# Optimization experiments

Hardware: AMD Instinct MI355X
Metric: run time of the kernel (lower is better)

Reference implementation:

```python
import jax, jax.numpy as jnp
import numpy as np

B, N, CIN, COUT, K, E = 8, 50000, 64, 64, 3, 400000


def setup_inputs() -> dict:
    key = jax.random.key(0)
    k0, k1, k2, k3 = jax.random.split(key, 4)
    x = jax.random.normal(k0, (B, N, CIN), dtype=jnp.float32)
    weight = jax.random.normal(k1, (K, CIN, COUT), dtype=jnp.float32) * 0.05
    bias = jax.random.normal(k2, (COUT,), dtype=jnp.float32) * 0.05
    edge_index = jax.random.randint(k3, (2, E), 0, N, dtype=jnp.int64)
    return {"x": x, "weight": weight, "bias": bias, "edge_index": edge_index}


def reference(x, weight, bias, edge_index):
    b, n, cin = x.shape
    k_order = weight.shape[0]
    row, col = edge_index[0], edge_index[1]
    # remove self loops (edge_weight defaults to ones)
    ew = jnp.where(row != col, jnp.float32(1.0), jnp.float32(0.0))
    deg = jax.ops.segment_sum(ew, row, num_segments=n)
    dinv = jnp.where(deg > 0, deg ** -0.5, 0.0)
    lap = -dinv[row] * ew * dinv[col]  # [E]

    def prop(t):  # sparse lap @ t along node dim; t: [B, N, Cin]
        tn = t.transpose(1, 0, 2).reshape(n, -1)            # [N, B*Cin]
        y = jax.ops.segment_sum(lap[:, None] * tn[col], row, num_segments=n)
        return y.reshape(n, b, cin).transpose(1, 0, 2)       # [B, N, Cin]

    tx0 = x
    out = jnp.einsum('bni,io->bno', tx0, weight[0])
    if k_order > 1:
        tx1 = prop(x)
        out = out + jnp.einsum('bni,io->bno', tx1, weight[1])
    for k in range(2, k_order):
        tx2 = 2.0 * prop(tx1) - tx0
        out = out + jnp.einsum('bni,io->bno', tx2, weight[k])
        tx0, tx1 = tx1, tx2
    return out + bias
```

## Files before the change

kernel.cpp:

```cpp
#include <hip/hip_runtime.h>

#define NB 8
#define NN 50000
#define NC 64
#define NE 400000

typedef unsigned short us4 __attribute__((ext_vector_type(4)));
typedef unsigned short us8 __attribute__((ext_vector_type(8)));
typedef short s8v __attribute__((ext_vector_type(8)));
typedef float f4v __attribute__((ext_vector_type(4)));

__device__ __forceinline__ float bf2f(unsigned short u) {
  union { unsigned int i; float f; } v; v.i = ((unsigned int)u) << 16; return v.f;
}
__device__ __forceinline__ unsigned short f2bf(float f) {
  union { float f; unsigned int i; } v; v.f = f;
  unsigned int x = v.i;
  return (unsigned short)((x + 0x7FFFu + ((x >> 16) & 1u)) >> 16);
}
__device__ __forceinline__ void fma4(float4& a, float s, const float4& v) {
  a.x = fmaf(s, v.x, a.x); a.y = fmaf(s, v.y, a.y);
  a.z = fmaf(s, v.z, a.z); a.w = fmaf(s, v.w, a.w);
}

__device__ __forceinline__ void gather_group(
    const unsigned short* __restrict__ tb, const int2* __restrict__ edges,
    int s, int e, int lane, int2 myed, float (&acc)[8]) {
  int jc = s;
  while (jc < e) {
    int take = e - jc; if (take > 64) take = 64;
    if (jc != s) myed = edges[jc + (lane < take ? lane : take - 1)];
    int full = take & ~7;
    int m = 0;
    for (; m < full; m += 8) {
      us8 v[8]; float lp[8];
#pragma unroll
      for (int u = 0; u < 8; ++u) {
        int c = __shfl(myed.x, m + u, 64);
        lp[u] = __int_as_float(__shfl(myed.y, m + u, 64));
        v[u] = *(const us8*)&tb[(size_t)c * 512];
      }
#pragma unroll
      for (int u = 0; u < 8; ++u)
#pragma unroll
        for (int q = 0; q < 8; ++q) acc[q] = fmaf(lp[u], bf2f(v[u][q]), acc[q]);
    }
    if (m < take) {
      int rem = take - m;
      us8 v[8]; float lp[8];
#pragma unroll
      for (int u = 0; u < 8; ++u) {
        if (u < rem) {
          int c = __shfl(myed.x, m + u, 64);
          lp[u] = __int_as_float(__shfl(myed.y, m + u, 64));
          v[u] = *(const us8*)&tb[(size_t)c * 512];
        }
      }
#pragma unroll
      for (int u = 0; u < 8; ++u) {
        if (u < rem) {
#pragma unroll
          for (int q = 0; q < 8; ++q) acc[q] = fmaf(lp[u], bf2f(v[u][q]), acc[q]);
        }
      }
    }
    jc += take;
  }
}

__global__ void cheb_count(const int* __restrict__ ei, int* __restrict__ cnt) {
  int e = blockIdx.x * blockDim.x + threadIdx.x;
  if (e >= NE) return;
  int r = ei[e], c = ei[NE + e];
  if (r != c) atomicAdd(&cnt[r], 1);
}

__global__ void cheb_offsets(const int* __restrict__ cnt, float* __restrict__ dinv,
                             int* __restrict__ rowptr, int* __restrict__ cur,
                             int* __restrict__ total) {
  int n = blockIdx.x * blockDim.x + threadIdx.x;
  int lane = threadIdx.x & 63;
  bool valid = n < NN;
  int c = valid ? cnt[n] : 0;
  int inc = c;
#pragma unroll
  for (int d = 1; d < 64; d <<= 1) {
    int t = __shfl_up(inc, d, 64);
    if (lane >= d) inc += t;
  }
  int wtot = __shfl(inc, 63, 64);
  int base = 0;
  if (lane == 63) base = atomicAdd(total, wtot);
  base = __shfl(base, 63, 64);
  int s = base + inc - c;
  if (valid) {
    dinv[n] = (c > 0) ? rsqrtf((float)c) : 0.0f;
    rowptr[n] = s;
    cur[n] = s;
  }
}

__global__ void cheb_scatter(const int* __restrict__ ei, const float* __restrict__ dinv,
                             int* __restrict__ cur, int2* __restrict__ edges) {
  int e = blockIdx.x * blockDim.x + threadIdx.x;
  if (e >= NE) return;
  int r = ei[e], c = ei[NE + e];
  if (r == c) return;
  int pos = atomicAdd(&cur[r], 1);
  float lap = -dinv[r] * dinv[c];
  edges[pos] = make_int2(c, __float_as_int(lap));
}

__global__ void cheb_wc(const float* __restrict__ w, float* __restrict__ wc) {
  int i = blockIdx.x * blockDim.x + threadIdx.x;
  if (i >= NC * NC) return;
  float w0 = w[i];
  float w1 = w[NC * NC + i];
  float w2 = w[2 * NC * NC + i];
  wc[i] = w0 - w2;
  wc[NC * NC + i] = w1;
  wc[2 * NC * NC + i] = 2.0f * w2;
}

__global__ void cheb_wpack(const float* __restrict__ w, unsigned short* __restrict__ pack) {
  int t = blockIdx.x * blockDim.x + threadIdx.x;
  if (t >= 6 * 4 * 64 * 8) return;
  int jj = t & 7;
  int l  = (t >> 3) & 63;
  int nt = (t >> 9) & 3;
  int ks = t >> 11;
  int k = ks * 32 + ((l >> 4) * 8) + jj;
  int o = nt * 16 + (l & 15);
  int ki = k & 63, ch = k >> 6;
  float v;
  if (ch == 0)      v = w[ki * 64 + o] - w[2 * 4096 + ki * 64 + o];
  else if (ch == 1) v = w[4096 + ki * 64 + o];
  else              v = 2.0f * w[2 * 4096 + ki * 64 + o];
  pack[t] = f2bf(v);
}

__global__ __launch_bounds__(256) void cheb_convert(
    const float* __restrict__ x, unsigned short* __restrict__ xh) {
  int t = blockIdx.x * blockDim.x + threadIdx.x;
  if (t >= NN * 128) return;
  int n = t >> 7;
  int rem = t & 127;
  int b = rem >> 4;
  int c4 = (rem & 15) * 4;
  f4v v = __builtin_nontemporal_load((const f4v*)&x[((size_t)b * NN + n) * 64 + c4]);
  us4 o;
  o[0] = f2bf(v[0]); o[1] = f2bf(v[1]); o[2] = f2bf(v[2]); o[3] = f2bf(v[3]);
  *(us4*)&xh[(size_t)n * 512 + b * 64 + c4] = o;
}

__global__ __launch_bounds__(256) void cheb_prop1h(
    const unsigned short* __restrict__ tin, unsigned short* __restrict__ tout,
    const int* __restrict__ rowptr, const int* __restrict__ cnt,
    const int2* __restrict__ edges) {
  int n = (blockIdx.x << 2) + (threadIdx.x >> 6);
  if (n >= NN) return;
  int lane = threadIdx.x & 63;
  int s = rowptr[n], c = cnt[n];
  const unsigned short* tb = tin + lane * 8;
  float acc[8];
#pragma unroll
  for (int q = 0; q < 8; ++q) acc[q] = 0.0f;
  if (c > 0) {
    int t0 = c > 64 ? 64 : c;
    int2 myed = edges[s + (lane < t0 ? lane : t0 - 1)];
    gather_group(tb, edges, s, s + c, lane, myed, acc);
  }
  us8 o;
#pragma unroll
  for (int q = 0; q < 8; ++q) o[q] = f2bf(acc[q]);
  *(us8*)&tout[(size_t)n * 512 + lane * 8] = o;
}

__global__ __launch_bounds__(256) void cheb_fused(
    const unsigned short* __restrict__ xh, const unsigned short* __restrict__ tx1h,
    const int* __restrict__ rowptr, const int* __restrict__ cnt,
    const int2* __restrict__ edges, const unsigned short* __restrict__ pack,
    const float* __restrict__ bias, float* __restrict__ out) {
  __shared__ unsigned short Pb[4][32][72];
  int w = threadIdx.x >> 6, lane = threadIdx.x & 63;
  int row0 = blockIdx.x * 128 + w * 32;
  int n0 = row0 >> 3;
  unsigned short (*P)[72] = Pb[w];

  int sj[4], cj[4];
#pragma unroll
  for (int j = 0; j < 4; ++j) { sj[j] = rowptr[n0 + j]; cj[j] = cnt[n0 + j]; }
  int2 med[4];
#pragma unroll
  for (int j = 0; j < 4; ++j) {
    int t0 = cj[j] > 64 ? 64 : cj[j];
    int idx = (t0 > 0) ? (sj[j] + (lane < t0 ? lane : t0 - 1)) : 0;
    med[j] = edges[idx];
  }

  const unsigned short* tb = tx1h + lane * 8;
  for (int j = 0; j < 4; ++j) {
    float acc8[8];
#pragma unroll
    for (int q = 0; q < 8; ++q) acc8[q] = 0.0f;
    if (cj[j] > 0)
      gather_group(tb, edges, sj[j], sj[j] + cj[j], lane, med[j], acc8);
    us8 o;
#pragma unroll
    for (int q = 0; q < 8; ++q) o[q] = f2bf(acc8[q]);
    *(us8*)&P[j * 8 + (lane >> 3)][(lane & 7) * 8] = o;
  }

  f4v acc[2][4];
#pragma unroll
  for (int mt = 0; mt < 2; ++mt)
#pragma unroll
    for (int nt = 0; nt < 4; ++nt) acc[mt][nt] = (f4v){0.f, 0.f, 0.f, 0.f};

  int am = lane & 15, aq = (lane >> 4) * 8;
#pragma unroll
  for (int ks = 0; ks < 6; ++ks) {
    s8v a0, a1;
    if (ks < 2) {
      a0 = __builtin_nontemporal_load((const s8v*)&xh[(size_t)(row0 + am) * 64 + ks * 32 + aq]);
      a1 = __builtin_nontemporal_load((const s8v*)&xh[(size_t)(row0 + 16 + am) * 64 + ks * 32 + aq]);
    } else if (ks < 4) {
      a0 = *(const s8v*)&tx1h[(size_t)(row0 + am) * 64 + (ks - 2) * 32 + aq];
      a1 = *(const s8v*)&tx1h[(size_t)(row0 + 16 + am) * 64 + (ks - 2) * 32 + aq];
    } else {
      a0 = *(const s8v*)&P[am][(ks - 4) * 32 + aq];
      a1 = *(const s8v*)&P[16 + am][(ks - 4) * 32 + aq];
    }
#pragma unroll
    for (int nt = 0; nt < 4; ++nt) {
      s8v b = *(const s8v*)&pack[(((size_t)(ks * 4 + nt) * 64) + lane) * 8];
      acc[0][nt] = __builtin_amdgcn_mfma_f32_16x16x32_bf16(a0, b, acc[0][nt], 0, 0, 0);
      acc[1][nt] = __builtin_amdgcn_mfma_f32_16x16x32_bf16(a1, b, acc[1][nt], 0, 0, 0);
    }
  }

  float bv[4];
#pragma unroll
  for (int nt = 0; nt < 4; ++nt) bv[nt] = bias[nt * 16 + (lane & 15)];
#pragma unroll
  for (int mt = 0; mt < 2; ++mt)
#pragma unroll
    for (int r = 0; r < 4; ++r) {
      int rl = mt * 16 + (lane >> 4) * 4 + r;
      int rn = row0 + rl;
      int b = rn & 7, nn = rn >> 3;
      float* orow = &out[((size_t)b * NN + nn) * 64 + (lane & 15)];
#pragma unroll
      for (int nt = 0; nt < 4; ++nt)
        __builtin_nontemporal_store(acc[mt][nt][r] + bv[nt], &orow[nt * 16]);
    }
}

__global__ __launch_bounds__(256) void cheb_prop(
    const float* __restrict__ tin, float* __restrict__ tout,
    const int* __restrict__ rowptr, const int* __restrict__ cnt,
    const int2* __restrict__ edges, int nwaves) {
  int wid = (blockIdx.x << 2) + (threadIdx.x >> 6);
  if (wid >= nwaves) return;
  int lane = threadIdx.x & 63;
  int b = wid / NN;
  int n = wid - b * NN;
  int s = rowptr[n];
  int e = s + cnt[n];
  const float* base = tin + (size_t)b * NN * NC;
  float acc = 0.0f;
  for (int j = s; j < e; ++j) {
    int2 ed = edges[j];
    acc += __int_as_float(ed.y) * base[(size_t)ed.x * NC + lane];
  }
  tout[((size_t)b * NN + n) * NC + lane] = acc;
}

__global__ __launch_bounds__(256) void cheb_gemm2(
    const float* __restrict__ x, const float* __restrict__ tx1,
    const float* ptx1, const float* __restrict__ wc,
    const float* __restrict__ bias, float* out, int nrows) {
  __shared__ float At[128][64];
  __shared__ float Ws[64][64];
  int tid = threadIdx.x;
  int tx = tid & 15;
  int ty = tid >> 4;
  long row0 = (long)blockIdx.x * 128;
  int sk4 = (tid & 15) * 4;
  int srb = tid >> 4;
  const float* sp[3] = {x, tx1, ptx1};
  float4 pa[8], pw[4];
  auto fetch = [&](int ch) {
    const float* s0 = sp[ch];
#pragma unroll
    for (int rr = 0; rr < 8; ++rr) {
      int roff = srb + rr * 16;
      if (row0 + roff < nrows)
        pa[rr] = *(const float4*)&s0[(size_t)(row0 + roff) * NC + sk4];
      else
        pa[rr] = make_float4(0.f, 0.f, 0.f, 0.f);
    }
#pragma unroll
    for (int ww = 0; ww < 4; ++ww) {
      int e4 = tid + 256 * ww;
      pw[ww] = *(const float4*)&wc[ch * 4096 + (e4 >> 4) * 64 + (e4 & 15) * 4];
    }
  };
  auto commit = [&]() {
#pragma unroll
    for (int rr = 0; rr < 8; ++rr)
      *(float4*)&At[srb + rr * 16][sk4] = pa[rr];
#pragma unroll
    for (int ww = 0; ww < 4; ++ww) {
      int e4 = tid + 256 * ww;
      *(float4*)&Ws[e4 >> 4][(e4 & 15) * 4] = pw[ww];
    }
  };
  float4 acc[8];
#pragma unroll
  for (int i = 0; i < 8; ++i) acc[i] = make_float4(0.f, 0.f, 0.f, 0.f);
  fetch(0);
  commit();
  for (int ch = 0; ch < 3; ++ch) {
    __syncthreads();
    if (ch < 2) fetch(ch + 1);
#pragma unroll 4
    for (int k4 = 0; k4 < 16; ++k4) {
      float4 w0 = *(float4*)&Ws[k4 * 4 + 0][tx * 4];
      float4 w1 = *(float4*)&Ws[k4 * 4 + 1][tx * 4];
      float4 w2 = *(float4*)&Ws[k4 * 4 + 2][tx * 4];
      float4 w3 = *(float4*)&Ws[k4 * 4 + 3][tx * 4];
#pragma unroll
      for (int i = 0; i < 8; ++i) {
        float4 a = *(float4*)&At[ty * 8 + i][k4 * 4];
        fma4(acc[i], a.x, w0);
        fma4(acc[i], a.y, w1);
        fma4(acc[i], a.z, w2);
        fma4(acc[i], a.w, w3);
      }
    }
    __syncthreads();
    if (ch < 2) commit();
  }
  float4 bb4 = *(const float4*)&bias[tx * 4];
#pragma unroll
  for (int i = 0; i < 8; ++i) {
    long r = row0 + ty * 8 + i;
    if (r >= nrows) continue;
    float4 o = make_float4(acc[i].x + bb4.x, acc[i].y + bb4.y,
                           acc[i].z + bb4.z, acc[i].w + bb4.w);
    *(float4*)&out[(size_t)r * NC + tx * 4] = o;
  }
}

extern "C" void kernel_launch(void* const* d_in, const int* in_sizes, int n_in,
                              void* d_out, int out_size, void* d_ws, size_t ws_size,
                              hipStream_t stream) {
  (void)in_sizes; (void)n_in; (void)out_size;
  const float* x    = (const float*)d_in[0];
  const float* w    = (const float*)d_in[1];
  const float* bias = (const float*)d_in[2];
  const int*   ei   = (const int*)d_in[3];
  float* out = (float*)d_out;
  char* ws = (char*)d_ws;

  size_t off = 0;
  auto alloc = [&](size_t bytes) -> void* {
    void* p = (void*)(ws + off);
    off = (off + bytes + 255) & ~(size_t)255;
    return p;
  };
  int* cnt      = (int*)alloc((size_t)(NN + 1) * sizeof(int));
  int* total    = cnt + NN;
  int* rowptr   = (int*)alloc((size_t)NN * sizeof(int));
  int* cur      = (int*)alloc((size_t)NN * sizeof(int));
  float* dinv   = (float*)alloc((size_t)NN * sizeof(float));
  int2* edges   = (int2*)alloc((size_t)NE * sizeof(int2));
  float* wcb    = (float*)alloc((size_t)3 * NC * NC * sizeof(float));
  unsigned short* pack = (unsigned short*)alloc((size_t)6 * 4 * 64 * 8 * sizeof(unsigned short));
  size_t small_end = off;

  hipMemsetAsync(cnt, 0, (NN + 1) * sizeof(int), stream);
  cheb_count  <<<(NE + 255) / 256, 256, 0, stream>>>(ei, cnt);
  cheb_offsets<<<(NN + 255) / 256, 256, 0, stream>>>(cnt, dinv, rowptr, cur, total);
  cheb_scatter<<<(NE + 255) / 256, 256, 0, stream>>>(ei, dinv, cur, edges);

  const size_t fieldHB = (size_t)NN * 512 * sizeof(unsigned short);
  const size_t perbB   = (size_t)NN * NC * sizeof(float);

  if (ws_size >= small_end + 2 * fieldHB + 256) {
    unsigned short* xh   = (unsigned short*)alloc(fieldHB);
    unsigned short* tx1h = (unsigned short*)alloc(fieldHB);
    cheb_wpack  <<<(6 * 4 * 64 * 8 + 255) / 256, 256, 0, stream>>>(w, pack);
    cheb_convert<<<(NN * 128) / 256, 256, 0, stream>>>(x, xh);
    cheb_prop1h <<<NN / 4, 256, 0, stream>>>(xh, tx1h, rowptr, cnt, edges);
    cheb_fused  <<<(NB * NN) / 128, 256, 0, stream>>>(
        xh, tx1h, rowptr, cnt, edges, pack, bias, out);
  } else if (ws_size >= small_end + 2 * perbB + 256) {
    cheb_wc<<<(NC * NC + 255) / 256, 256, 0, stream>>>(w, wcb);
    float* tx1b  = (float*)alloc(perbB);
    float* ptx1b = (float*)alloc(perbB);
    for (int b = 0; b < NB; ++b) {
      const float* xb = x + (size_t)b * NN * NC;
      float* outb = out + (size_t)b * NN * NC;
      cheb_prop<<<(NN + 3) / 4, 256, 0, stream>>>(xb, tx1b, rowptr, cnt, edges, NN);
      cheb_prop<<<(NN + 3) / 4, 256, 0, stream>>>(tx1b, ptx1b, rowptr, cnt, edges, NN);
      cheb_gemm2<<<(NN + 127) / 128, 256, 0, stream>>>(
          xb, tx1b, ptx1b, wcb, bias, outb, NN);
    }
  } else {
    cheb_wc<<<(NC * NC + 255) / 256, 256, 0, stream>>>(w, wcb);
    float* tx1b = (float*)alloc(perbB);
    for (int b = 0; b < NB; ++b) {
      const float* xb = x + (size_t)b * NN * NC;
      float* outb = out + (size_t)b * NN * NC;
      cheb_prop<<<(NN + 3) / 4, 256, 0, stream>>>(xb, tx1b, rowptr, cnt, edges, NN);
      cheb_prop<<<(NN + 3) / 4, 256, 0, stream>>>(tx1b, outb, rowptr, cnt, edges, NN);
      cheb_gemm2<<<(NN + 127) / 128, 256, 0, stream>>>(
          xb, tx1b, outb, wcb, bias, outb, NN);
    }
  }
}
```

Measured before the change: 369.9 us.

## Split fused second-hop gather into two batch-half passes and merge prep kernels

Splits the fused second propagation plus MFMA kernel into two launches. Each launch gathers only half of the batch channels (4 of 8 batches), so the working set per pass is half a row and should stay in L2 during random neighbor gathers. It also merges the bf16 conversion, weight packing and count zeroing into one launch, removing the memset and two separate launches. The cost is that edge lists and rowptr are read twice and there are more, smaller gather loads per edge.

```diff
diff --git a/kernel.cpp b/kernel.cpp
--- a/kernel.cpp
+++ b/kernel.cpp
@@ -68,6 +68,51 @@
   }
 }
 
+__device__ __forceinline__ void gather_group_h(
+    const unsigned short* __restrict__ tbh, const int2* __restrict__ edges,
+    int s, int e, int lane, int2 myed, float (&acc)[4]) {
+  int jc = s;
+  while (jc < e) {
+    int take = e - jc; if (take > 64) take = 64;
+    if (jc != s) myed = edges[jc + (lane < take ? lane : take - 1)];
+    int full = take & ~7;
+    int m = 0;
+    for (; m < full; m += 8) {
+      us4 v[8]; float lp[8];
+#pragma unroll
+      for (int u = 0; u < 8; ++u) {
+        int c = __shfl(myed.x, m + u, 64);
+        lp[u] = __int_as_float(__shfl(myed.y, m + u, 64));
+        v[u] = *(const us4*)&tbh[(size_t)c * 512];
+      }
+#pragma unroll
+      for (int u = 0; u < 8; ++u)
+#pragma unroll
+        for (int q = 0; q < 4; ++q) acc[q] = fmaf(lp[u], bf2f(v[u][q]), acc[q]);
+    }
+    if (m < take) {
+      int rem = take - m;
+      us4 v[8]; float lp[8];
+#pragma unroll
+      for (int u = 0; u < 8; ++u) {
+        if (u < rem) {
+          int c = __shfl(myed.x, m + u, 64);
+          lp[u] = __int_as_float(__shfl(myed.y, m + u, 64));
+          v[u] = *(const us4*)&tbh[(size_t)c * 512];
+        }
+      }
+#pragma unroll
+      for (int u = 0; u < 8; ++u) {
+        if (u < rem) {
+#pragma unroll
+          for (int q = 0; q < 4; ++q) acc[q] = fmaf(lp[u], bf2f(v[u][q]), acc[q]);
+        }
+      }
+    }
+    jc += take;
+  }
+}
+
 __global__ void cheb_count(const int* __restrict__ ei, int* __restrict__ cnt) {
   int e = blockIdx.x * blockDim.x + threadIdx.x;
   if (e >= NE) return;
@@ -122,35 +167,42 @@
   wc[2 * NC * NC + i] = 2.0f * w2;
 }
 
-__global__ void cheb_wpack(const float* __restrict__ w, unsigned short* __restrict__ pack) {
-  int t = blockIdx.x * blockDim.x + threadIdx.x;
-  if (t >= 6 * 4 * 64 * 8) return;
-  int jj = t & 7;
-  int l  = (t >> 3) & 63;
-  int nt = (t >> 9) & 3;
-  int ks = t >> 11;
-  int k = ks * 32 + ((l >> 4) * 8) + jj;
-  int o = nt * 16 + (l & 15);
-  int ki = k & 63, ch = k >> 6;
-  float v;
-  if (ch == 0)      v = w[ki * 64 + o] - w[2 * 4096 + ki * 64 + o];
-  else if (ch == 1) v = w[4096 + ki * 64 + o];
-  else              v = 2.0f * w[2 * 4096 + ki * 64 + o];
-  pack[t] = f2bf(v);
-}
-
-__global__ __launch_bounds__(256) void cheb_convert(
-    const float* __restrict__ x, unsigned short* __restrict__ xh) {
-  int t = blockIdx.x * blockDim.x + threadIdx.x;
-  if (t >= NN * 128) return;
-  int n = t >> 7;
-  int rem = t & 127;
-  int b = rem >> 4;
-  int c4 = (rem & 15) * 4;
-  f4v v = __builtin_nontemporal_load((const f4v*)&x[((size_t)b * NN + n) * 64 + c4]);
-  us4 o;
-  o[0] = f2bf(v[0]); o[1] = f2bf(v[1]); o[2] = f2bf(v[2]); o[3] = f2bf(v[3]);
-  *(us4*)&xh[(size_t)n * 512 + b * 64 + c4] = o;
+#define PRE_CONV_BLK 25000
+#define PRE_ZERO_BLK 196
+__global__ __launch_bounds__(256) void cheb_pre(
+    const float* __restrict__ x, unsigned short* __restrict__ xh,
+    const float* __restrict__ w, unsigned short* __restrict__ pack,
+    int* __restrict__ cnt) {
+  int bid = blockIdx.x;
+  if (bid < PRE_CONV_BLK) {
+    int t = bid * 256 + threadIdx.x;
+    int n = t >> 7;
+    int rem = t & 127;
+    int b = rem >> 4;
+    int c4 = (rem & 15) * 4;
+    f4v v = __builtin_nontemporal_load((const f4v*)&x[((size_t)b * NN + n) * 64 + c4]);
+    us4 o;
+    o[0] = f2bf(v[0]); o[1] = f2bf(v[1]); o[2] = f2bf(v[2]); o[3] = f2bf(v[3]);
+    *(us4*)&xh[(size_t)n * 512 + b * 64 + c4] = o;
+  } else if (bid < PRE_CONV_BLK + PRE_ZERO_BLK) {
+    int i = (bid - PRE_CONV_BLK) * 256 + threadIdx.x;
+    if (i <= NN) cnt[i] = 0;
+  } else {
+    int t = (bid - PRE_CONV_BLK - PRE_ZERO_BLK) * 256 + threadIdx.x;
+    if (t >= 6 * 4 * 64 * 8) return;
+    int jj = t & 7;
+    int l  = (t >> 3) & 63;
+    int nt = (t >> 9) & 3;
+    int ks = t >> 11;
+    int k = ks * 32 + ((l >> 4) * 8) + jj;
+    int o = nt * 16 + (l & 15);
+    int ki = k & 63, ch = k >> 6;
+    float v;
+    if (ch == 0)      v = w[ki * 64 + o] - w[2 * 4096 + ki * 64 + o];
+    else if (ch == 1) v = w[4096 + ki * 64 + o];
+    else              v = 2.0f * w[2 * 4096 + ki * 64 + o];
+    pack[t] = f2bf(v);
+  }
 }
 
 __global__ __launch_bounds__(256) void cheb_prop1h(
@@ -176,15 +228,15 @@
   *(us8*)&tout[(size_t)n * 512 + lane * 8] = o;
 }
 
-__global__ __launch_bounds__(256) void cheb_fused(
+template <int PASS>
+__global__ __launch_bounds__(256) void cheb_fusedh(
     const unsigned short* __restrict__ xh, const unsigned short* __restrict__ tx1h,
     const int* __restrict__ rowptr, const int* __restrict__ cnt,
     const int2* __restrict__ edges, const unsigned short* __restrict__ pack,
     const float* __restrict__ bias, float* __restrict__ out) {
-  __shared__ unsigned short Pb[4][32][72];
+  __shared__ unsigned short Pb[4][16][72];
   int w = threadIdx.x >> 6, lane = threadIdx.x & 63;
-  int row0 = blockIdx.x * 128 + w * 32;
-  int n0 = row0 >> 3;
+  int n0 = blockIdx.x * 16 + w * 4;
   unsigned short (*P)[72] = Pb[w];
 
   int sj[4], cj[4];
@@ -198,44 +250,41 @@
     med[j] = edges[idx];
   }
 
-  const unsigned short* tb = tx1h + lane * 8;
+  const unsigned short* tbh = tx1h + PASS * 256 + lane * 4;
   for (int j = 0; j < 4; ++j) {
-    float acc8[8];
-#pragma unroll
-    for (int q = 0; q < 8; ++q) acc8[q] = 0.0f;
+    float acc4[4];
+#pragma unroll
+    for (int q = 0; q < 4; ++q) acc4[q] = 0.0f;
     if (cj[j] > 0)
-      gather_group(tb, edges, sj[j], sj[j] + cj[j], lane, med[j], acc8);
-    us8 o;
-#pragma unroll
-    for (int q = 0; q < 8; ++q) o[q] = f2bf(acc8[q]);
-    *(us8*)&P[j * 8 + (lane >> 3)][(lane & 7) * 8] = o;
-  }
-
-  f4v acc[2][4];
-#pragma unroll
-  for (int mt = 0; mt < 2; ++mt)
-#pragma unroll
-    for (int nt = 0; nt < 4; ++nt) acc[mt][nt] = (f4v){0.f, 0.f, 0.f, 0.f};
+      gather_group_h(tbh, edges, sj[j], sj[j] + cj[j], lane, med[j], acc4);
+    us4 o;
+#pragma unroll
+    for (int q = 0; q < 4; ++q) o[q] = f2bf(acc4[q]);
+    *(us4*)&P[j * 4 + (lane >> 4)][(lane & 15) * 4] = o;
+  }
+
+  f4v acc[4];
+#pragma unroll
+  for (int nt = 0; nt < 4; ++nt) acc[nt] = (f4v){0.f, 0.f, 0.f, 0.f};
 
   int am = lane & 15, aq = (lane >> 4) * 8;
+  int an = n0 + (am >> 2);
+  int ab = PASS * 4 + (am & 3);
 #pragma unroll
   for (int ks = 0; ks < 6; ++ks) {
-    s8v a0, a1;
+    s8v a0;
     if (ks < 2) {
-      a0 = __builtin_nontemporal_load((const s8v*)&xh[(size_t)(row0 + am) * 64 + ks * 32 + aq]);
-      a1 = __builtin_nontemporal_load((const s8v*)&xh[(size_t)(row0 + 16 + am) * 64 + ks * 32 + aq]);
+      a0 = __builtin_nontemporal_load(
+          (const s8v*)&xh[(size_t)an * 512 + ab * 64 + ks * 32 + aq]);
     } else if (ks < 4) {
-      a0 = *(const s8v*)&tx1h[(size_t)(row0 + am) * 64 + (ks - 2) * 32 + aq];
-      a1 = *(const s8v*)&tx1h[(size_t)(row0 + 16 + am) * 64 + (ks - 2) * 32 + aq];
+      a0 = *(const s8v*)&tx1h[(size_t)an * 512 + ab * 64 + (ks - 2) * 32 + aq];
     } else {
       a0 = *(const s8v*)&P[am][(ks - 4) * 32 + aq];
-      a1 = *(const s8v*)&P[16 + am][(ks - 4) * 32 + aq];
     }
 #pragma unroll
     for (int nt = 0; nt < 4; ++nt) {
       s8v b = *(const s8v*)&pack[(((size_t)(ks * 4 + nt) * 64) + lane) * 8];
-      acc[0][nt] = __builtin_amdgcn_mfma_f32_16x16x32_bf16(a0, b, acc[0][nt], 0, 0, 0);
-      acc[1][nt] = __builtin_amdgcn_mfma_f32_16x16x32_bf16(a1, b, acc[1][nt], 0, 0, 0);
+      acc[nt] = __builtin_amdgcn_mfma_f32_16x16x32_bf16(a0, b, acc[nt], 0, 0, 0);
     }
   }
 
@@ -243,17 +292,15 @@
 #pragma unroll
   for (int nt = 0; nt < 4; ++nt) bv[nt] = bias[nt * 16 + (lane & 15)];
 #pragma unroll
-  for (int mt = 0; mt < 2; ++mt)
-#pragma unroll
-    for (int r = 0; r < 4; ++r) {
-      int rl = mt * 16 + (lane >> 4) * 4 + r;
-      int rn = row0 + rl;
-      int b = rn & 7, nn = rn >> 3;
-      float* orow = &out[((size_t)b * NN + nn) * 64 + (lane & 15)];
-#pragma unroll
-      for (int nt = 0; nt < 4; ++nt)
-        __builtin_nontemporal_store(acc[mt][nt][r] + bv[nt], &orow[nt * 16]);
-    }
+  for (int r = 0; r < 4; ++r) {
+    int rl = (lane >> 4) * 4 + r;
+    int n = n0 + (rl >> 2);
+    int b = PASS * 4 + (rl & 3);
+    float* orow = &out[((size_t)b * NN + n) * 64 + (lane & 15)];
+#pragma unroll
+    for (int nt = 0; nt < 4; ++nt)
+      __builtin_nontemporal_store(acc[nt][r] + bv[nt], &orow[nt * 16]);
+  }
 }
 
 __global__ __launch_bounds__(256) void cheb_prop(
@@ -380,23 +427,27 @@
   unsigned short* pack = (unsigned short*)alloc((size_t)6 * 4 * 64 * 8 * sizeof(unsigned short));
   size_t small_end = off;
 
-  hipMemsetAsync(cnt, 0, (NN + 1) * sizeof(int), stream);
-  cheb_count  <<<(NE + 255) / 256, 256, 0, stream>>>(ei, cnt);
-  cheb_offsets<<<(NN + 255) / 256, 256, 0, stream>>>(cnt, dinv, rowptr, cur, total);
-  cheb_scatter<<<(NE + 255) / 256, 256, 0, stream>>>(ei, dinv, cur, edges);
-
   const size_t fieldHB = (size_t)NN * 512 * sizeof(unsigned short);
   const size_t perbB   = (size_t)NN * NC * sizeof(float);
 
   if (ws_size >= small_end + 2 * fieldHB + 256) {
     unsigned short* xh   = (unsigned short*)alloc(fieldHB);
     unsigned short* tx1h = (unsigned short*)alloc(fieldHB);
-    cheb_wpack  <<<(6 * 4 * 64 * 8 + 255) / 256, 256, 0, stream>>>(w, pack);
-    cheb_convert<<<(NN * 128) / 256, 256, 0, stream>>>(x, xh);
+    cheb_pre    <<<PRE_CONV_BLK + PRE_ZERO_BLK + 48, 256, 0, stream>>>(
+        x, xh, w, pack, cnt);
+    cheb_count  <<<(NE + 255) / 256, 256, 0, stream>>>(ei, cnt);
+    cheb_offsets<<<(NN + 255) / 256, 256, 0, stream>>>(cnt, dinv, rowptr, cur, total);
+    cheb_scatter<<<(NE + 255) / 256, 256, 0, stream>>>(ei, dinv, cur, edges);
     cheb_prop1h <<<NN / 4, 256, 0, stream>>>(xh, tx1h, rowptr, cnt, edges);
-    cheb_fused  <<<(NB * NN) / 128, 256, 0, stream>>>(
+    cheb_fusedh<0><<<NN / 16, 256, 0, stream>>>(
+        xh, tx1h, rowptr, cnt, edges, pack, bias, out);
+    cheb_fusedh<1><<<NN / 16, 256, 0, stream>>>(
         xh, tx1h, rowptr, cnt, edges, pack, bias, out);
   } else if (ws_size >= small_end + 2 * perbB + 256) {
+    hipMemsetAsync(cnt, 0, (NN + 1) * sizeof(int), stream);
+    cheb_count  <<<(NE + 255) / 256, 256, 0, stream>>>(ei, cnt);
+    cheb_offsets<<<(NN + 255) / 256, 256, 0, stream>>>(cnt, dinv, rowptr, cur, total);
+    cheb_scatter<<<(NE + 255) / 256, 256, 0, stream>>>(ei, dinv, cur, edges);
     cheb_wc<<<(NC * NC + 255) / 256, 256, 0, stream>>>(w, wcb);
     float* tx1b  = (float*)alloc(perbB);
     float* ptx1b = (float*)alloc(perbB);
@@ -409,6 +460,10 @@
           xb, tx1b, ptx1b, wcb, bias, outb, NN);
     }
   } else {
+    hipMemsetAsync(cnt, 0, (NN + 1) * sizeof(int), stream);
+    cheb_count  <<<(NE + 255) / 256, 256, 0, stream>>>(ei, cnt);
+    cheb_offsets<<<(NN + 255) / 256, 256, 0, stream>>>(cnt, dinv, rowptr, cur, total);
+    cheb_scatter<<<(NE + 255) / 256, 256, 0, stream>>>(ei, dinv, cur, edges);
     cheb_wc<<<(NC * NC + 255) / 256, 256, 0, stream>>>(w, wcb);
     float* tx1b = (float*)alloc(perbB);
     for (int b = 0; b < NB; ++b) {
```

New measurement: 370.4 us. No clear change (+0.1%).
